# Performance work log

Measured on AMD Instinct MI355X. Metric: run time of the kernel, lower is better.

The kernel has to match this reference:

```python
import jax, jax.numpy as jnp
import numpy as np

FS = 16000
TAU_R = 0.002
TAU_ST = 0.06
KERNEL_DUR = 0.3
K = int(KERNEL_DUR * FS)  # 4800 taps


def _build_kernel(dtype):
    # double-exponential adaptation kernel, normalized to unit sum
    t = jnp.arange(K, dtype=dtype) / FS
    k = jnp.exp(-t / TAU_R) + jnp.exp(-t / TAU_ST)
    return k / k.sum()


def setup_inputs() -> dict:
    key = jax.random.key(0)
    x = jax.random.normal(key, (8, 64, 48000), dtype=jnp.float32)
    return {"x": x}


def reference(x):
    # x: (B, C, T) -> (B, C, T + K - 1)
    B, C, T = x.shape
    x = jax.nn.softplus(x)
    kern = jnp.broadcast_to(_build_kernel(x.dtype), (C, 1, K))  # (O=C, I/g=1, K)
    # torch F.conv1d is cross-correlation with padding=K-1 on both sides (full conv)
    y = jax.lax.conv_general_dilated(
        x, kern,
        window_strides=(1,),
        padding=[(K - 1, K - 1)],
        dimension_numbers=("NCH", "OIH", "NCH"),
        feature_group_count=C,
    )
    return y
```

## Files before the change

kernel.cpp:

```cpp
#include <hip/hip_runtime.h>
#include <math.h>


#define TT    48000
#define KK    4800
#define OUTT  52799
#define SEGS  8
#define LSEG  6656
#define HALO  6144
#define TILE  512
#define NT    ((LSEG + HALO) / TILE)
#define NST   (LSEG / TILE)
#define SMIN  (48000 - SEGS * LSEG)

__device__ __forceinline__ float softplus_fast(float v) {
    const float t = __expf(-fabsf(v));
    return fmaxf(v, 0.0f) + __logf(1.0f + t);
}

__device__ __forceinline__ void ld8sp(float o[8], const float* __restrict__ base, int s) {
    if (s >= 0 && s + 8 <= TT) {
        const float4 v0 = *reinterpret_cast<const float4*>(base + s);
        const float4 v1 = *reinterpret_cast<const float4*>(base + s + 4);
        o[0] = v0.x; o[1] = v0.y; o[2] = v0.z; o[3] = v0.w;
        o[4] = v1.x; o[5] = v1.y; o[6] = v1.z; o[7] = v1.w;
        #pragma unroll
        for (int j = 0; j < 8; ++j) o[j] = softplus_fast(o[j]);
    } else {
        #pragma unroll
        for (int j = 0; j < 8; ++j) {
            const int ss = s + j;
            o[j] = (ss >= 0 && ss < TT) ? softplus_fast(base[ss]) : 0.0f;
        }
    }
}

__global__ __launch_bounds__(256) void dtca_fused_kernel(
    const float* __restrict__ x, float* __restrict__ y,
    float a1, float a2, float c2, float invS, int nch)
{
    const int wid  = blockIdx.x * 4 + (threadIdx.x >> 6);
    const int lane = threadIdx.x & 63;
    const int ch   = wid >> 3;
    const int seg  = wid & 7;
    if (ch >= nch) return;

    const float* __restrict__ xc = x + (size_t)ch * TT;
    float* __restrict__ yc       = y + (size_t)ch * OUTT;
    const int segLo = SMIN + seg * LSEG;

    float p1[9], p2[9];
    p1[0] = 1.0f; p2[0] = 1.0f;
    #pragma unroll
    for (int k = 1; k <= 8; ++k) { p1[k] = p1[k - 1] * a1; p2[k] = p2[k - 1] * a2; }
    const float A1 = p1[8], A2 = p2[8];
    const float P1 = powf(a1, (float)(512 - 8 * lane));
    const float P2 = powf(a2, (float)(512 - 8 * lane));

    float pc1 = 0.0f, pc2 = 0.0f;

    for (int t = NT - 1; t >= 0; --t) {
        const int sBase = segLo + t * TILE;
        const int s0 = sBase + 8 * lane;

        float xs[8], xk[8];
        ld8sp(xs, xc, s0);
        ld8sp(xk, xc, s0 + KK);

        float L1[8], L2[8];
        float h1 = 0.0f, h2 = 0.0f;
        #pragma unroll
        for (int j = 7; j >= 0; --j) {
            const float u2 = fmaf(-c2, xk[j], xs[j]);
            h1 = fmaf(a1, h1, xs[j]); L1[j] = h1;
            h2 = fmaf(a2, h2, u2);    L2[j] = h2;
        }

        float s1 = L1[0], s2 = L2[0];
        float f1 = A1, f2 = A2;
        #pragma unroll
        for (int d = 1; d < 64; d <<= 1) {
            float v1 = __shfl_down(s1, d);
            float v2 = __shfl_down(s2, d);
            if (lane + d >= 64) { v1 = 0.0f; v2 = 0.0f; }
            s1 = fmaf(f1, v1, s1);
            s2 = fmaf(f2, v2, s2);
            f1 *= f1; f2 *= f2;
        }
        const float S1 = fmaf(P1, pc1, s1);
        const float S2 = fmaf(P2, pc2, s2);
        float cin1 = __shfl_down(S1, 1);
        float cin2 = __shfl_down(S2, 1);
        if (lane == 63) { cin1 = pc1; cin2 = pc2; }
        pc1 = __shfl(S1, 0);
        pc2 = __shfl(S2, 0);

        if (t < NST) {
            float out[8];
            out[0] = (S1 + S2) * invS;
            #pragma unroll
            for (int j = 1; j < 8; ++j) {
                const float g1 = fmaf(p1[8 - j], cin1, L1[j]);
                const float g2 = fmaf(p2[8 - j], cin2, L2[j]);
                out[j] = (g1 + g2) * invS;
            }
            const int t0 = s0 + (KK - 1);
            if (t0 >= 0) {
                #pragma unroll
                for (int j = 0; j < 8; ++j) yc[t0 + j] = out[j];
            } else {
                #pragma unroll
                for (int j = 0; j < 8; ++j) if (t0 + j >= 0) yc[t0 + j] = out[j];
            }
        }
    }
}

extern "C" void kernel_launch(void* const* d_in, const int* in_sizes, int n_in,
                              void* d_out, int out_size, void* d_ws, size_t ws_size,
                              hipStream_t stream) {
    const float* x = (const float*)d_in[0];
    float* y = (float*)d_out;

    const int nelem = in_sizes[0];
    const int nch   = nelem / TT;

    const double a1d = exp(-1.0 / 32.0);
    const double a2d = exp(-1.0 / 960.0);
    const double c1d = exp(-4800.0 / 32.0);
    const double c2d = exp(-4800.0 / 960.0);
    const double S   = (1.0 - c1d) / (1.0 - a1d) + (1.0 - c2d) / (1.0 - a2d);

    const float a1 = (float)a1d, a2 = (float)a2d;
    const float c2 = (float)c2d, invS = (float)(1.0 / S);

    const int scanBlocks = (nch * SEGS * 64 + 255) / 256;
    dtca_fused_kernel<<<scanBlocks, 256, 0, stream>>>(
        x, y, a1, a2, c2, invS, nch);
}
```

Baseline: 224.6 us.

## Replace second input load with register ring of delayed scan states

The kernel no longer reloads x at offset K for the truncated slow exponential. It keeps the slow-scan results from five tiles earlier (TILE*5 = K) in a register ring buffer packed as bf16 pairs, and subtracts c2 times that delayed value. Tiles are retiled to 960 samples with 15 elements per lane and 5 segments per channel, one block of 5 waves per channel. The change halves global input loads and softplus evaluations at the cost of bf16 precision in the correction term, more registers, and fewer, larger blocks.

Measured after the change: 205.6 us. 1.09x faster.

```diff
diff --git a/kernel.cpp b/kernel.cpp
--- a/kernel.cpp
+++ b/kernel.cpp
@@ -1,119 +1,171 @@
 #include <hip/hip_runtime.h>
+#include <hip/hip_bf16.h>
 #include <math.h>
 
 
 #define TT    48000
 #define KK    4800
 #define OUTT  52799
-#define SEGS  8
-#define LSEG  6656
-#define HALO  6144
-#define TILE  512
-#define NT    ((LSEG + HALO) / TILE)
-#define NST   (LSEG / TILE)
-#define SMIN  (48000 - SEGS * LSEG)
+#define SEGS  5
+#define E     15
+#define TILE  960
+#define NSTT  11
+#define LSEG  (NSTT * TILE)
+#define NT    16
+#define RD    5
+#define SMIN  (TT - SEGS * LSEG)
 
 __device__ __forceinline__ float softplus_fast(float v) {
-    const float t = __expf(-fabsf(v));
-    return fmaxf(v, 0.0f) + __logf(1.0f + t);
+    return __logf(1.0f + __expf(v));
 }
 
-__device__ __forceinline__ void ld8sp(float o[8], const float* __restrict__ base, int s) {
-    if (s >= 0 && s + 8 <= TT) {
-        const float4 v0 = *reinterpret_cast<const float4*>(base + s);
-        const float4 v1 = *reinterpret_cast<const float4*>(base + s + 4);
-        o[0] = v0.x; o[1] = v0.y; o[2] = v0.z; o[3] = v0.w;
-        o[4] = v1.x; o[5] = v1.y; o[6] = v1.z; o[7] = v1.w;
+__device__ __forceinline__ unsigned pack_bf2(float a, float b) {
+    union { __hip_bfloat16 h; unsigned short u; } ca, cb;
+    ca.h = __float2bfloat16(a);
+    cb.h = __float2bfloat16(b);
+    return (unsigned)ca.u | ((unsigned)cb.u << 16);
+}
+
+__device__ __forceinline__ float2 unpack_bf2(unsigned v) {
+    union { unsigned u; float f; } fa, fb;
+    fa.u = (v & 0xffffu) << 16;
+    fb.u = v & 0xffff0000u;
+    return make_float2(fa.f, fb.f);
+}
+
+template <int SLOT, bool STORES>
+__device__ __forceinline__ void tile_step(
+    int tau, int segTop, int lane,
+    const float* __restrict__ xc, float* __restrict__ yc,
+    float a1, float a2, float c2, float invS,
+    const float (&p1)[E + 1], const float (&p2)[E + 1],
+    float P1, float P2,
+    float& pc1, float& pc2,
+    unsigned (&ring)[RD][8])
+{
+    const int sLow = segTop - (tau + 1) * TILE;
+    const int s0 = sLow + E * lane;
+
+    float xs[E];
+    if (s0 >= 0 && s0 + E <= TT) {
         #pragma unroll
-        for (int j = 0; j < 8; ++j) o[j] = softplus_fast(o[j]);
+        for (int j = 0; j < E; ++j) xs[j] = softplus_fast(xc[s0 + j]);
     } else {
         #pragma unroll
-        for (int j = 0; j < 8; ++j) {
-            const int ss = s + j;
-            o[j] = (ss >= 0 && ss < TT) ? softplus_fast(base[ss]) : 0.0f;
+        for (int j = 0; j < E; ++j) {
+            const int ss = s0 + j;
+            xs[j] = (ss >= 0 && ss < TT) ? softplus_fast(xc[ss]) : 0.0f;
         }
     }
+
+    float L1[E], L2[E];
+    float h1 = 0.0f, h2 = 0.0f;
+    #pragma unroll
+    for (int j = E - 1; j >= 0; --j) {
+        h1 = fmaf(a1, h1, xs[j]); L1[j] = h1;
+        h2 = fmaf(a2, h2, xs[j]); L2[j] = h2;
+    }
+
+    float sc1 = L1[0], sc2 = L2[0];
+    float f1 = p1[E], f2 = p2[E];
+    #pragma unroll
+    for (int d = 1; d < 64; d <<= 1) {
+        float v1 = __shfl_down(sc1, d);
+        float v2 = __shfl_down(sc2, d);
+        if (lane + d >= 64) { v1 = 0.0f; v2 = 0.0f; }
+        sc1 = fmaf(f1, v1, sc1);
+        sc2 = fmaf(f2, v2, sc2);
+        f1 *= f1; f2 *= f2;
+    }
+    const float S1 = fmaf(P1, pc1, sc1);
+    const float S2 = fmaf(P2, pc2, sc2);
+    float cin1 = __shfl_down(S1, 1);
+    float cin2 = __shfl_down(S2, 1);
+    if (lane == 63) { cin1 = pc1; cin2 = pc2; }
+    pc1 = __shfl(S1, 0);
+    pc2 = __shfl(S2, 0);
+
+    float g2v[16];
+    #pragma unroll
+    for (int j = 0; j < E; ++j) g2v[j] = fmaf(p2[E - j], cin2, L2[j]);
+    g2v[15] = 0.0f;
+
+    if (STORES) {
+        float old[16];
+        #pragma unroll
+        for (int p = 0; p < 8; ++p) {
+            const float2 f = unpack_bf2(ring[SLOT][p]);
+            old[2 * p] = f.x; old[2 * p + 1] = f.y;
+        }
+        const int t0 = s0 + (KK - 1);
+        float out[E];
+        #pragma unroll
+        for (int j = 0; j < E; ++j) {
+            const float g1 = fmaf(p1[E - j], cin1, L1[j]);
+            out[j] = (g1 + g2v[j] - c2 * old[j]) * invS;
+        }
+        if (t0 >= 0) {
+            #pragma unroll
+            for (int j = 0; j < E; ++j) yc[t0 + j] = out[j];
+        } else {
+            #pragma unroll
+            for (int j = 0; j < E; ++j) if (t0 + j >= 0) yc[t0 + j] = out[j];
+        }
+    }
+
+    #pragma unroll
+    for (int p = 0; p < 8; ++p)
+        ring[SLOT][p] = pack_bf2(g2v[2 * p], g2v[2 * p + 1]);
 }
 
-__global__ __launch_bounds__(256) void dtca_fused_kernel(
+__global__ __launch_bounds__(320) void dtca_ring_kernel(
     const float* __restrict__ x, float* __restrict__ y,
-    float a1, float a2, float c2, float invS, int nch)
+    float a1, float a2, float c2, float invS)
 {
-    const int wid  = blockIdx.x * 4 + (threadIdx.x >> 6);
+    const int ch   = blockIdx.x;
+    const int seg  = threadIdx.x >> 6;
     const int lane = threadIdx.x & 63;
-    const int ch   = wid >> 3;
-    const int seg  = wid & 7;
-    if (ch >= nch) return;
 
     const float* __restrict__ xc = x + (size_t)ch * TT;
     float* __restrict__ yc       = y + (size_t)ch * OUTT;
-    const int segLo = SMIN + seg * LSEG;
 
-    float p1[9], p2[9];
+    const int segLo  = SMIN + seg * LSEG;
+    const int segTop = segLo + NT * TILE;
+
+    float p1[E + 1], p2[E + 1];
     p1[0] = 1.0f; p2[0] = 1.0f;
     #pragma unroll
-    for (int k = 1; k <= 8; ++k) { p1[k] = p1[k - 1] * a1; p2[k] = p2[k - 1] * a2; }
-    const float A1 = p1[8], A2 = p2[8];
-    const float P1 = powf(a1, (float)(512 - 8 * lane));
-    const float P2 = powf(a2, (float)(512 - 8 * lane));
+    for (int k = 1; k <= E; ++k) { p1[k] = p1[k - 1] * a1; p2[k] = p2[k - 1] * a2; }
+    const float P1 = __powf(a1, (float)(TILE - E * lane));
+    const float P2 = __powf(a2, (float)(TILE - E * lane));
+
+    unsigned ring[RD][8];
+    #pragma unroll
+    for (int r = 0; r < RD; ++r)
+        #pragma unroll
+        for (int p = 0; p < 8; ++p) ring[r][p] = 0u;
 
     float pc1 = 0.0f, pc2 = 0.0f;
 
-    for (int t = NT - 1; t >= 0; --t) {
-        const int sBase = segLo + t * TILE;
-        const int s0 = sBase + 8 * lane;
+    #define TSTEP(SL, ST, TAU) \
+        tile_step<SL, ST>(TAU, segTop, lane, xc, yc, a1, a2, c2, invS, \
+                          p1, p2, P1, P2, pc1, pc2, ring)
 
-        float xs[8], xk[8];
-        ld8sp(xs, xc, s0);
-        ld8sp(xk, xc, s0 + KK);
-
-        float L1[8], L2[8];
-        float h1 = 0.0f, h2 = 0.0f;
-        #pragma unroll
-        for (int j = 7; j >= 0; --j) {
-            const float u2 = fmaf(-c2, xk[j], xs[j]);
-            h1 = fmaf(a1, h1, xs[j]); L1[j] = h1;
-            h2 = fmaf(a2, h2, u2);    L2[j] = h2;
-        }
-
-        float s1 = L1[0], s2 = L2[0];
-        float f1 = A1, f2 = A2;
-        #pragma unroll
-        for (int d = 1; d < 64; d <<= 1) {
-            float v1 = __shfl_down(s1, d);
-            float v2 = __shfl_down(s2, d);
-            if (lane + d >= 64) { v1 = 0.0f; v2 = 0.0f; }
-            s1 = fmaf(f1, v1, s1);
-            s2 = fmaf(f2, v2, s2);
-            f1 *= f1; f2 *= f2;
-        }
-        const float S1 = fmaf(P1, pc1, s1);
-        const float S2 = fmaf(P2, pc2, s2);
-        float cin1 = __shfl_down(S1, 1);
-        float cin2 = __shfl_down(S2, 1);
-        if (lane == 63) { cin1 = pc1; cin2 = pc2; }
-        pc1 = __shfl(S1, 0);
-        pc2 = __shfl(S2, 0);
-
-        if (t < NST) {
-            float out[8];
-            out[0] = (S1 + S2) * invS;
-            #pragma unroll
-            for (int j = 1; j < 8; ++j) {
-                const float g1 = fmaf(p1[8 - j], cin1, L1[j]);
-                const float g2 = fmaf(p2[8 - j], cin2, L2[j]);
-                out[j] = (g1 + g2) * invS;
-            }
-            const int t0 = s0 + (KK - 1);
-            if (t0 >= 0) {
-                #pragma unroll
-                for (int j = 0; j < 8; ++j) yc[t0 + j] = out[j];
-            } else {
-                #pragma unroll
-                for (int j = 0; j < 8; ++j) if (t0 + j >= 0) yc[t0 + j] = out[j];
-            }
-        }
+    TSTEP(0, false, 0);
+    TSTEP(1, false, 1);
+    TSTEP(2, false, 2);
+    TSTEP(3, false, 3);
+    TSTEP(4, false, 4);
+    for (int g = 1; g <= 2; ++g) {
+        const int t5 = 5 * g;
+        TSTEP(0, true, t5 + 0);
+        TSTEP(1, true, t5 + 1);
+        TSTEP(2, true, t5 + 2);
+        TSTEP(3, true, t5 + 3);
+        TSTEP(4, true, t5 + 4);
     }
+    TSTEP(0, true, 15);
+    #undef TSTEP
 }
 
 extern "C" void kernel_launch(void* const* d_in, const int* in_sizes, int n_in,
@@ -131,10 +183,6 @@
     const double c2d = exp(-4800.0 / 960.0);
     const double S   = (1.0 - c1d) / (1.0 - a1d) + (1.0 - c2d) / (1.0 - a2d);
 
-    const float a1 = (float)a1d, a2 = (float)a2d;
-    const float c2 = (float)c2d, invS = (float)(1.0 / S);
-
-    const int scanBlocks = (nch * SEGS * 64 + 255) / 256;
-    dtca_fused_kernel<<<scanBlocks, 256, 0, stream>>>(
-        x, y, a1, a2, c2, invS, nch);
+    dtca_ring_kernel<<<nch, 320, 0, stream>>>(
+        x, y, (float)a1d, (float)a2d, (float)c2d, (float)(1.0 / S));
 }
```
